# Kernel optimization log

Measured on AMD Instinct MI355X. Metric: run time of the kernel, lower is better.

The kernel has to match this reference:

```python
import jax, jax.numpy as jnp
import numpy as np

P = 1048576      # number of sampled ray points
H = 524288       # number of sparse voxels
NEMB = 600000    # number of corner embeddings (total_num_embedding)
D = 32           # voxel_embed_dim
VOXEL_SIZE = 0.25


def setup_inputs() -> dict:
    key = jax.random.key(0)
    k1, k2, k3, k4, k5 = jax.random.split(key, 5)
    point_xyz = jax.random.normal(k1, (H, 3), dtype=jnp.float32) * 5.0
    values = jax.random.normal(k2, (NEMB, D), dtype=jnp.float32)
    sampled_idx = jax.random.randint(k3, (P,), 0, H, dtype=jnp.int64)
    point_feats = jax.random.randint(k4, (H, 8), 0, NEMB, dtype=jnp.int64)
    # sample points lie inside their voxel (realistic, keeps interp weights in [0,1])
    jitter = (jax.random.uniform(k5, (P, 3), dtype=jnp.float32) - 0.5) * VOXEL_SIZE
    sampled_xyz = point_xyz[sampled_idx] + jitter
    return {
        "sampled_xyz": sampled_xyz,
        "point_xyz": point_xyz,
        "values": values,
        "sampled_idx": sampled_idx,
        "point_feats": point_feats,
    }


def _corner_q(dtype):
    # offset_points(p, 0.5, offset_only=True) + 0.5 -> {0,1}^3 corners, torch 'ij' meshgrid order
    c = jnp.arange(2)
    q = jnp.stack(jnp.meshgrid(c, c, c, indexing="ij"), axis=-1).reshape(8, 3)
    return q.astype(dtype)  # [8,3]


def reference(sampled_xyz, point_xyz, values, sampled_idx, point_feats):
    # gather per-sample voxel center and its 8 corner embedding ids
    pxyz = point_xyz[sampled_idx]        # [P,3]
    pf = point_feats[sampled_idx]        # [P,8]
    feats = values[pf]                   # [P,8,D]  (F.embedding)
    # normalized position inside voxel, in [0,1]^3
    p = (sampled_xyz - pxyz) / VOXEL_SIZE + 0.5   # [P,3]
    q = _corner_q(p.dtype)                        # [8,3]
    # trilinear weights: prod over xyz of (p*q + (1-p)*(1-q))
    w = jnp.prod(p[:, None, :] * q[None] + (1.0 - p[:, None, :]) * (1.0 - q[None]), axis=-1)  # [P,8]
    return jnp.einsum("pc,pcd->pd", w, feats)     # [P,D]
```

## Files before the change

kernel.cpp:

```cpp
#include <hip/hip_runtime.h>


#define VOXEL_INV 4.0f

typedef float vfloat4 __attribute__((ext_vector_type(4)));

__global__ __launch_bounds__(256) void svenc_kernel(
    const float* __restrict__ sampled_xyz,
    const float* __restrict__ point_xyz,
    const float* __restrict__ values,
    const int*   __restrict__ sampled_idx,
    const int*   __restrict__ point_feats,
    float*       __restrict__ out,
    int P)
{
    int t   = blockIdx.x * blockDim.x + threadIdx.x;
    int pid = t >> 3;
    int sub = t & 7;
    if (pid >= P) return;

    int vi = __builtin_nontemporal_load(sampled_idx + pid);

    float sx = __builtin_nontemporal_load(sampled_xyz + pid * 3 + 0);
    float sy = __builtin_nontemporal_load(sampled_xyz + pid * 3 + 1);
    float sz = __builtin_nontemporal_load(sampled_xyz + pid * 3 + 2);

    float cx = point_xyz[(size_t)vi * 3 + 0];
    float cy = point_xyz[(size_t)vi * 3 + 1];
    float cz = point_xyz[(size_t)vi * 3 + 2];

    float px = (sx - cx) * VOXEL_INV + 0.5f;
    float py = (sy - cy) * VOXEL_INV + 0.5f;
    float pz = (sz - cz) * VOXEL_INV + 0.5f;

    float xs[2] = {1.0f - px, px};
    float ys[2] = {1.0f - py, py};
    float zs[2] = {1.0f - pz, pz};

    const int4* pf4 = (const int4*)(point_feats + ((size_t)vi << 3));
    int4 f0 = pf4[0];
    int4 f1 = pf4[1];
    int ids[8] = {f0.x, f0.y, f0.z, f0.w, f1.x, f1.y, f1.z, f1.w};

    vfloat4 acc = {0.0f, 0.0f, 0.0f, 0.0f};
#pragma unroll
    for (int c = 0; c < 8; ++c) {
        float w = xs[(c >> 2) & 1] * ys[(c >> 1) & 1] * zs[c & 1];
        const vfloat4 v = ((const vfloat4*)(values + ((size_t)ids[c] << 5)))[sub];
        acc += w * v;
    }

    __builtin_nontemporal_store(acc, (vfloat4*)(out + ((size_t)pid << 5)) + sub);
}

extern "C" void kernel_launch(void* const* d_in, const int* in_sizes, int n_in,
                              void* d_out, int out_size, void* d_ws, size_t ws_size,
                              hipStream_t stream) {
    const float* sampled_xyz = (const float*)d_in[0];
    const float* point_xyz   = (const float*)d_in[1];
    const float* values      = (const float*)d_in[2];
    const int*   sampled_idx = (const int*)d_in[3];
    const int*   point_feats = (const int*)d_in[4];
    float* out = (float*)d_out;

    int P = in_sizes[3];
    long total_threads = (long)P * 8;
    int block = 256;
    int grid = (int)((total_threads + block - 1) / block);

    svenc_kernel<<<grid, block, 0, stream>>>(
        sampled_xyz, point_xyz, values, sampled_idx, point_feats, out, P);
}
```

Before: 378.0 us.

## Bucket samples by voxel to reuse corner embeddings across samples

Adds a counting sort of samples by voxel index: a histogram with atomics, a three-stage prefix scan and an atomic scatter into a permutation. A per-voxel kernel then loads the 8 corner embedding rows once and applies them to every sample in that voxel. The aim is to cut the random gather traffic from the 600K×32 value table, since each voxel is hit by about two samples on average. In exchange it adds several extra launches, global atomics and an indirect permutation read. Voxels with many samples also create load imbalance within a wave. The old direct kernel is kept as a fallback when the workspace is too small.

Measured after the change: 417.8 us. +10.5%, slower.

```diff
diff --git a/kernel.cpp b/kernel.cpp
--- a/kernel.cpp
+++ b/kernel.cpp
@@ -5,7 +5,7 @@
 
 typedef float vfloat4 __attribute__((ext_vector_type(4)));
 
-__global__ __launch_bounds__(256) void svenc_kernel(
+__global__ __launch_bounds__(256) void svenc_direct(
     const float* __restrict__ sampled_xyz,
     const float* __restrict__ point_xyz,
     const float* __restrict__ values,
@@ -49,8 +49,151 @@
         const vfloat4 v = ((const vfloat4*)(values + ((size_t)ids[c] << 5)))[sub];
         acc += w * v;
     }
-
     __builtin_nontemporal_store(acc, (vfloat4*)(out + ((size_t)pid << 5)) + sub);
+}
+
+__global__ __launch_bounds__(256) void k_hist(
+    const int* __restrict__ idx, int* __restrict__ counts, int P)
+{
+    int p = blockIdx.x * 256 + threadIdx.x;
+    if (p < P) atomicAdd(&counts[idx[p]], 1);
+}
+
+__global__ __launch_bounds__(256) void k_scan_a(
+    const int* __restrict__ counts, int* __restrict__ blockSums, int H)
+{
+    __shared__ int s[256];
+    int b = blockIdx.x, tid = threadIdx.x;
+    int base = b * 2048 + tid * 8;
+    int sum = 0;
+    if (base + 8 <= H) {
+        const int4* c4 = (const int4*)(counts + base);
+        int4 a = c4[0], bb = c4[1];
+        sum = a.x + a.y + a.z + a.w + bb.x + bb.y + bb.z + bb.w;
+    } else {
+        for (int j = 0; j < 8; ++j) if (base + j < H) sum += counts[base + j];
+    }
+    s[tid] = sum; __syncthreads();
+    for (int off = 128; off > 0; off >>= 1) {
+        if (tid < off) s[tid] += s[tid + off];
+        __syncthreads();
+    }
+    if (tid == 0) blockSums[b] = s[0];
+}
+
+__global__ __launch_bounds__(256) void k_scan_b(
+    const int* __restrict__ blockSums, int* __restrict__ blockBase, int nb)
+{
+    __shared__ int s[256];
+    int tid = threadIdx.x;
+    int v = (tid < nb) ? blockSums[tid] : 0;
+    s[tid] = v; __syncthreads();
+    for (int off = 1; off < 256; off <<= 1) {
+        int t = (tid >= off) ? s[tid - off] : 0;
+        __syncthreads();
+        s[tid] += t;
+        __syncthreads();
+    }
+    if (tid < nb) blockBase[tid] = s[tid] - v;
+}
+
+__global__ __launch_bounds__(256) void k_scan_c(
+    const int* __restrict__ counts, const int* __restrict__ blockBase,
+    int* __restrict__ offsets, int* __restrict__ cursor, int H)
+{
+    __shared__ int s[256];
+    int b = blockIdx.x, tid = threadIdx.x;
+    int base = b * 2048 + tid * 8;
+    int c[8]; int sum = 0;
+#pragma unroll
+    for (int j = 0; j < 8; ++j) {
+        int h = base + j;
+        c[j] = (h < H) ? counts[h] : 0;
+        sum += c[j];
+    }
+    s[tid] = sum; __syncthreads();
+    for (int off = 1; off < 256; off <<= 1) {
+        int t = (tid >= off) ? s[tid - off] : 0;
+        __syncthreads();
+        s[tid] += t;
+        __syncthreads();
+    }
+    int run = blockBase[b] + s[tid] - sum;
+#pragma unroll
+    for (int j = 0; j < 8; ++j) {
+        int h = base + j;
+        if (h < H) { offsets[h] = run; cursor[h] = run; run += c[j]; }
+    }
+}
+
+__global__ __launch_bounds__(256) void k_scatter(
+    const int* __restrict__ idx, int* __restrict__ cursor,
+    int* __restrict__ perm, int P)
+{
+    int p = blockIdx.x * 256 + threadIdx.x;
+    if (p < P) {
+        int pos = atomicAdd(&cursor[idx[p]], 1);
+        perm[pos] = p;
+    }
+}
+
+__global__ __launch_bounds__(256) void svenc_voxel(
+    const float* __restrict__ sampled_xyz,
+    const float* __restrict__ point_xyz,
+    const float* __restrict__ values,
+    const int*   __restrict__ point_feats,
+    const int*   __restrict__ offsets,
+    const int*   __restrict__ counts,
+    const int*   __restrict__ perm,
+    float*       __restrict__ out,
+    int H)
+{
+    int t   = blockIdx.x * 256 + threadIdx.x;
+    int g   = t >> 3;
+    int sub = t & 7;
+    if (g >= H) return;
+
+    int n = counts[g];
+    if (n == 0) return;
+    int start = offsets[g];
+
+    float cx = point_xyz[(size_t)g * 3 + 0];
+    float cy = point_xyz[(size_t)g * 3 + 1];
+    float cz = point_xyz[(size_t)g * 3 + 2];
+
+    const int4* pf4 = (const int4*)(point_feats + ((size_t)g << 3));
+    int4 f0 = pf4[0];
+    int4 f1 = pf4[1];
+    int ids[8] = {f0.x, f0.y, f0.z, f0.w, f1.x, f1.y, f1.z, f1.w};
+
+    vfloat4 v[8];
+#pragma unroll
+    for (int c = 0; c < 8; ++c)
+        v[c] = ((const vfloat4*)(values + ((size_t)ids[c] << 5)))[sub];
+
+    for (int i = 0; i < n; ++i) {
+        int p = perm[start + i];
+
+        float sx = sampled_xyz[(size_t)p * 3 + 0];
+        float sy = sampled_xyz[(size_t)p * 3 + 1];
+        float sz = sampled_xyz[(size_t)p * 3 + 2];
+
+        float px = (sx - cx) * VOXEL_INV + 0.5f;
+        float py = (sy - cy) * VOXEL_INV + 0.5f;
+        float pz = (sz - cz) * VOXEL_INV + 0.5f;
+
+        float xs[2] = {1.0f - px, px};
+        float ys[2] = {1.0f - py, py};
+        float zs[2] = {1.0f - pz, pz};
+
+        vfloat4 acc = {0.0f, 0.0f, 0.0f, 0.0f};
+#pragma unroll
+        for (int c = 0; c < 8; ++c) {
+            float w = xs[(c >> 2) & 1] * ys[(c >> 1) & 1] * zs[c & 1];
+            acc += w * v[c];
+        }
+        __builtin_nontemporal_store(acc, (vfloat4*)(out + ((size_t)p << 5)) + sub);
+    }
 }
 
 extern "C" void kernel_launch(void* const* d_in, const int* in_sizes, int n_in,
@@ -64,10 +207,44 @@
     float* out = (float*)d_out;
 
     int P = in_sizes[3];
-    long total_threads = (long)P * 8;
-    int block = 256;
-    int grid = (int)((total_threads + block - 1) / block);
-
-    svenc_kernel<<<grid, block, 0, stream>>>(
-        sampled_xyz, point_xyz, values, sampled_idx, point_feats, out, P);
-}
+
+    int H;
+    if (in_sizes[0] == 3 * P)       H = in_sizes[4] / 8;
+    else                            H = in_sizes[4];
+
+    int nb = (H + 2047) / 2048;
+    size_t need_ints = (size_t)3 * H + 512 + (size_t)P;
+    bool sorted_ok = (d_ws != nullptr) && (ws_size >= need_ints * 4) &&
+                     (H > 0) && (nb <= 256);
+
+    if (!sorted_ok) {
+        long total_threads = (long)P * 8;
+        int grid = (int)((total_threads + 255) / 256);
+        svenc_direct<<<grid, 256, 0, stream>>>(
+            sampled_xyz, point_xyz, values, sampled_idx, point_feats, out, P);
+        return;
+    }
+
+    int* ws        = (int*)d_ws;
+    int* counts    = ws;
+    int* blockSums = ws + H;
+    int* blockBase = ws + H + 256;
+    int* offsets   = ws + H + 512;
+    int* cursor    = ws + 2 * (size_t)H + 512;
+    int* perm      = ws + 3 * (size_t)H + 512;
+
+    hipMemsetAsync(counts, 0, (size_t)H * 4, stream);
+
+    int gp = (P + 255) / 256;
+    k_hist   <<<gp, 256, 0, stream>>>(sampled_idx, counts, P);
+    k_scan_a <<<nb, 256, 0, stream>>>(counts, blockSums, H);
+    k_scan_b <<<1,  256, 0, stream>>>(blockSums, blockBase, nb);
+    k_scan_c <<<nb, 256, 0, stream>>>(counts, blockBase, offsets, cursor, H);
+    k_scatter<<<gp, 256, 0, stream>>>(sampled_idx, cursor, perm, P);
+
+    long tt = (long)H * 8;
+    int grid = (int)((tt + 255) / 256);
+    svenc_voxel<<<grid, 256, 0, stream>>>(
+        sampled_xyz, point_xyz, values, point_feats,
+        offsets, counts, perm, out, H);
+}
```

## Bucket samples by voxel to reuse corner embedding loads across samples

Applied to the files above, without the earlier changes.

Adds a bucketing pass that atomically groups sample indices (and optionally xyz) per voxel into a fixed-capacity workspace. A second kernel then loads each voxel's 8 corner embeddings once and applies them to every sample in its bucket. Overflow samples beyond capacity are computed directly. The aim is to cut redundant random gathers from the values table, since about 2 samples share each voxel. In exchange it adds a memset, atomics, a workspace round trip, and scattered output writes. The direct fallback still runs when no workspace is available.

Result: no change. 371.3 us (-1.8%).

```diff
diff --git a/kernel.cpp b/kernel.cpp
--- a/kernel.cpp
+++ b/kernel.cpp
@@ -2,10 +2,56 @@
 
 
 #define VOXEL_INV 4.0f
+#define CAP 8
 
 typedef float vfloat4 __attribute__((ext_vector_type(4)));
 
-__global__ __launch_bounds__(256) void svenc_kernel(
+__device__ __forceinline__ void corner_ids(const int* __restrict__ point_feats,
+                                           int vi, int* ids)
+{
+    const int4* pf4 = (const int4*)(point_feats + ((size_t)vi << 3));
+    int4 f0 = pf4[0];
+    int4 f1 = pf4[1];
+    ids[0] = f0.x; ids[1] = f0.y; ids[2] = f0.z; ids[3] = f0.w;
+    ids[4] = f1.x; ids[5] = f1.y; ids[6] = f1.z; ids[7] = f1.w;
+}
+
+__device__ void compute_point_direct(
+    const float* __restrict__ point_xyz,
+    const float* __restrict__ values,
+    const int*   __restrict__ point_feats,
+    float*       __restrict__ out,
+    int vi, int p, float sx, float sy, float sz)
+{
+    float cx = point_xyz[(size_t)vi * 3 + 0];
+    float cy = point_xyz[(size_t)vi * 3 + 1];
+    float cz = point_xyz[(size_t)vi * 3 + 2];
+
+    float px = (sx - cx) * VOXEL_INV + 0.5f;
+    float py = (sy - cy) * VOXEL_INV + 0.5f;
+    float pz = (sz - cz) * VOXEL_INV + 0.5f;
+
+    float xs[2] = {1.0f - px, px};
+    float ys[2] = {1.0f - py, py};
+    float zs[2] = {1.0f - pz, pz};
+
+    int ids[8];
+    corner_ids(point_feats, vi, ids);
+
+    vfloat4 acc[8] = {};
+#pragma unroll
+    for (int c = 0; c < 8; ++c) {
+        float w = xs[(c >> 2) & 1] * ys[(c >> 1) & 1] * zs[c & 1];
+        const vfloat4* vr = (const vfloat4*)(values + ((size_t)ids[c] << 5));
+#pragma unroll
+        for (int k = 0; k < 8; ++k) acc[k] += w * vr[k];
+    }
+    vfloat4* o = (vfloat4*)(out + ((size_t)p << 5));
+#pragma unroll
+    for (int k = 0; k < 8; ++k) __builtin_nontemporal_store(acc[k], o + k);
+}
+
+__global__ __launch_bounds__(256) void svenc_direct(
     const float* __restrict__ sampled_xyz,
     const float* __restrict__ point_xyz,
     const float* __restrict__ values,
@@ -20,7 +66,6 @@
     if (pid >= P) return;
 
     int vi = __builtin_nontemporal_load(sampled_idx + pid);
-
     float sx = __builtin_nontemporal_load(sampled_xyz + pid * 3 + 0);
     float sy = __builtin_nontemporal_load(sampled_xyz + pid * 3 + 1);
     float sz = __builtin_nontemporal_load(sampled_xyz + pid * 3 + 2);
@@ -37,10 +82,8 @@
     float ys[2] = {1.0f - py, py};
     float zs[2] = {1.0f - pz, pz};
 
-    const int4* pf4 = (const int4*)(point_feats + ((size_t)vi << 3));
-    int4 f0 = pf4[0];
-    int4 f1 = pf4[1];
-    int ids[8] = {f0.x, f0.y, f0.z, f0.w, f1.x, f1.y, f1.z, f1.w};
+    int ids[8];
+    corner_ids(point_feats, vi, ids);
 
     vfloat4 acc = {0.0f, 0.0f, 0.0f, 0.0f};
 #pragma unroll
@@ -49,8 +92,171 @@
         const vfloat4 v = ((const vfloat4*)(values + ((size_t)ids[c] << 5)))[sub];
         acc += w * v;
     }
-
     __builtin_nontemporal_store(acc, (vfloat4*)(out + ((size_t)pid << 5)) + sub);
+}
+
+__global__ __launch_bounds__(256) void k_bucket_xyz(
+    const float* __restrict__ sampled_xyz,
+    const float* __restrict__ point_xyz,
+    const float* __restrict__ values,
+    const int*   __restrict__ sampled_idx,
+    const int*   __restrict__ point_feats,
+    float*       __restrict__ out,
+    int*         __restrict__ counts,
+    vfloat4*     __restrict__ bucket,
+    int P)
+{
+    int p = blockIdx.x * 256 + threadIdx.x;
+    if (p >= P) return;
+
+    int vi = sampled_idx[p];
+    float sx = sampled_xyz[(size_t)p * 3 + 0];
+    float sy = sampled_xyz[(size_t)p * 3 + 1];
+    float sz = sampled_xyz[(size_t)p * 3 + 2];
+
+    int pos = atomicAdd(counts + vi, 1);
+    if (pos < CAP) {
+        vfloat4 e;
+        e.x = __int_as_float(p);
+        e.y = sx; e.z = sy; e.w = sz;
+        bucket[((size_t)vi << 3) + pos] = e;
+    } else {
+        compute_point_direct(point_xyz, values, point_feats, out, vi, p, sx, sy, sz);
+    }
+}
+
+__global__ __launch_bounds__(256) void svenc_voxel_xyz(
+    const float* __restrict__ point_xyz,
+    const float* __restrict__ values,
+    const int*   __restrict__ point_feats,
+    const int*   __restrict__ counts,
+    const vfloat4* __restrict__ bucket,
+    float*       __restrict__ out,
+    int H)
+{
+    int t   = blockIdx.x * 256 + threadIdx.x;
+    int g   = t >> 3;
+    int sub = t & 7;
+    if (g >= H) return;
+
+    int n = counts[g];
+    if (n == 0) return;
+    if (n > CAP) n = CAP;
+
+    float cx = point_xyz[(size_t)g * 3 + 0];
+    float cy = point_xyz[(size_t)g * 3 + 1];
+    float cz = point_xyz[(size_t)g * 3 + 2];
+
+    int ids[8];
+    corner_ids(point_feats, g, ids);
+
+    vfloat4 v[8];
+#pragma unroll
+    for (int c = 0; c < 8; ++c)
+        v[c] = ((const vfloat4*)(values + ((size_t)ids[c] << 5)))[sub];
+
+    for (int i = 0; i < n; ++i) {
+        vfloat4 e = bucket[((size_t)g << 3) + i];
+        int p = __float_as_int(e.x);
+
+        float px = (e.y - cx) * VOXEL_INV + 0.5f;
+        float py = (e.z - cy) * VOXEL_INV + 0.5f;
+        float pz = (e.w - cz) * VOXEL_INV + 0.5f;
+
+        float xs[2] = {1.0f - px, px};
+        float ys[2] = {1.0f - py, py};
+        float zs[2] = {1.0f - pz, pz};
+
+        vfloat4 acc = {0.0f, 0.0f, 0.0f, 0.0f};
+#pragma unroll
+        for (int c = 0; c < 8; ++c) {
+            float w = xs[(c >> 2) & 1] * ys[(c >> 1) & 1] * zs[c & 1];
+            acc += w * v[c];
+        }
+        __builtin_nontemporal_store(acc, (vfloat4*)(out + ((size_t)p << 5)) + sub);
+    }
+}
+
+__global__ __launch_bounds__(256) void k_bucket_id(
+    const float* __restrict__ sampled_xyz,
+    const float* __restrict__ point_xyz,
+    const float* __restrict__ values,
+    const int*   __restrict__ sampled_idx,
+    const int*   __restrict__ point_feats,
+    float*       __restrict__ out,
+    int*         __restrict__ counts,
+    int*         __restrict__ bucket,
+    int P)
+{
+    int p = blockIdx.x * 256 + threadIdx.x;
+    if (p >= P) return;
+
+    int vi = sampled_idx[p];
+    int pos = atomicAdd(counts + vi, 1);
+    if (pos < CAP) {
+        bucket[((size_t)vi << 3) + pos] = p;
+    } else {
+        float sx = sampled_xyz[(size_t)p * 3 + 0];
+        float sy = sampled_xyz[(size_t)p * 3 + 1];
+        float sz = sampled_xyz[(size_t)p * 3 + 2];
+        compute_point_direct(point_xyz, values, point_feats, out, vi, p, sx, sy, sz);
+    }
+}
+
+__global__ __launch_bounds__(256) void svenc_voxel_id(
+    const float* __restrict__ sampled_xyz,
+    const float* __restrict__ point_xyz,
+    const float* __restrict__ values,
+    const int*   __restrict__ point_feats,
+    const int*   __restrict__ counts,
+    const int*   __restrict__ bucket,
+    float*       __restrict__ out,
+    int H)
+{
+    int t   = blockIdx.x * 256 + threadIdx.x;
+    int g   = t >> 3;
+    int sub = t & 7;
+    if (g >= H) return;
+
+    int n = counts[g];
+    if (n == 0) return;
+    if (n > CAP) n = CAP;
+
+    float cx = point_xyz[(size_t)g * 3 + 0];
+    float cy = point_xyz[(size_t)g * 3 + 1];
+    float cz = point_xyz[(size_t)g * 3 + 2];
+
+    int ids[8];
+    corner_ids(point_feats, g, ids);
+
+    vfloat4 v[8];
+#pragma unroll
+    for (int c = 0; c < 8; ++c)
+        v[c] = ((const vfloat4*)(values + ((size_t)ids[c] << 5)))[sub];
+
+    for (int i = 0; i < n; ++i) {
+        int p = bucket[((size_t)g << 3) + i];
+
+        float sx = sampled_xyz[(size_t)p * 3 + 0];
+        float sy = sampled_xyz[(size_t)p * 3 + 1];
+        float sz = sampled_xyz[(size_t)p * 3 + 2];
+
+        float px = (sx - cx) * VOXEL_INV + 0.5f;
+        float py = (sy - cy) * VOXEL_INV + 0.5f;
+        float pz = (sz - cz) * VOXEL_INV + 0.5f;
+
+        float xs[2] = {1.0f - px, px};
+        float ys[2] = {1.0f - py, py};
+        float zs[2] = {1.0f - pz, pz};
+
+        vfloat4 acc = {0.0f, 0.0f, 0.0f, 0.0f};
+#pragma unroll
+        for (int c = 0; c < 8; ++c) {
+            float w = xs[(c >> 2) & 1] * ys[(c >> 1) & 1] * zs[c & 1];
+            acc += w * v[c];
+        }
+        __builtin_nontemporal_store(acc, (vfloat4*)(out + ((size_t)p << 5)) + sub);
+    }
 }
 
 extern "C" void kernel_launch(void* const* d_in, const int* in_sizes, int n_in,
@@ -64,10 +270,42 @@
     float* out = (float*)d_out;
 
     int P = in_sizes[3];
-    long total_threads = (long)P * 8;
-    int block = 256;
-    int grid = (int)((total_threads + block - 1) / block);
-
-    svenc_kernel<<<grid, block, 0, stream>>>(
-        sampled_xyz, point_xyz, values, sampled_idx, point_feats, out, P);
-}
+
+    int H;
+    if (in_sizes[0] == 3 * P)       H = in_sizes[4] / 8;
+    else                            H = in_sizes[4];
+
+    size_t bucketB_xyz = (size_t)H * CAP * 16;
+    size_t need_xyz    = bucketB_xyz + (size_t)H * 4;
+    size_t bucketB_id  = (size_t)H * CAP * 4;
+    size_t need_id     = bucketB_id + (size_t)H * 4;
+
+    int gp = (P + 255) / 256;
+    long tt = (long)H * 8;
+    int gm = (int)((tt + 255) / 256);
+
+    if (d_ws != nullptr && ws_size >= need_xyz && H > 0) {
+        vfloat4* bucket = (vfloat4*)d_ws;
+        int* counts = (int*)((char*)d_ws + bucketB_xyz);
+        hipMemsetAsync(counts, 0, (size_t)H * 4, stream);
+        k_bucket_xyz<<<gp, 256, 0, stream>>>(
+            sampled_xyz, point_xyz, values, sampled_idx, point_feats,
+            out, counts, bucket, P);
+        svenc_voxel_xyz<<<gm, 256, 0, stream>>>(
+            point_xyz, values, point_feats, counts, bucket, out, H);
+    } else if (d_ws != nullptr && ws_size >= need_id && H > 0) {
+        int* bucket = (int*)d_ws;
+        int* counts = (int*)((char*)d_ws + bucketB_id);
+        hipMemsetAsync(counts, 0, (size_t)H * 4, stream);
+        k_bucket_id<<<gp, 256, 0, stream>>>(
+            sampled_xyz, point_xyz, values, sampled_idx, point_feats,
+            out, counts, bucket, P);
+        svenc_voxel_id<<<gm, 256, 0, stream>>>(
+            sampled_xyz, point_xyz, values, point_feats, counts, bucket, out, H);
+    } else {
+        long total_threads = (long)P * 8;
+        int grid = (int)((total_threads + 255) / 256);
+        svenc_direct<<<grid, 256, 0, stream>>>(
+            sampled_xyz, point_xyz, values, sampled_idx, point_feats, out, P);
+    }
+}
```
